# Kernel tuning notes

Hardware: AMD Instinct MI355X
Metric: run time of the kernel (lower is better)

The kernel has to match this reference:

```python
import jax, jax.numpy as jnp
import numpy as np

B = 16384
WIDE_DIM = 256          # 32 wide features * dim 8
DEEP_DIM = 1024         # 64 deep features * embedding_dim 16
SHARED = [2048, 1024, 512]
DOMAIN = [512, 256]
NUM_DOMAINS = 8


def setup_inputs() -> dict:
    key = jax.random.key(0)
    ks = jax.random.split(key, 20)
    s = 0.01  # embedding_init_var-style small init
    inp = {
        "wide_features": jax.random.normal(ks[0], (B, WIDE_DIM), jnp.float32),
        "deep_features": jax.random.normal(ks[1], (B, DEEP_DIM), jnp.float32),
        "domain_ids": jax.random.randint(ks[2], (B,), 0, NUM_DOMAINS, jnp.int64),
        # shared MLP (weights stored [in, out])
        "W1": jax.random.normal(ks[3], (DEEP_DIM, SHARED[0]), jnp.float32) * s,
        "b1": jnp.zeros((SHARED[0],), jnp.float32),
        "W2": jax.random.normal(ks[4], (SHARED[0], SHARED[1]), jnp.float32) * s,
        "b2": jnp.zeros((SHARED[1],), jnp.float32),
        "W3": jax.random.normal(ks[5], (SHARED[1], SHARED[2]), jnp.float32) * s,
        "b3": jnp.zeros((SHARED[2],), jnp.float32),
        # domain-specific MLP
        "Wd1": jax.random.normal(ks[6], (SHARED[2], DOMAIN[0]), jnp.float32) * s,
        "bd1": jnp.zeros((DOMAIN[0],), jnp.float32),
        "Wd2": jax.random.normal(ks[7], (DOMAIN[0], DOMAIN[1]), jnp.float32) * s,
        "bd2": jnp.zeros((DOMAIN[1],), jnp.float32),
        # per-domain output heads: Linear(DOMAIN[-1], 1) per domain
        "Wh": jax.random.normal(ks[8], (NUM_DOMAINS, DOMAIN[1]), jnp.float32) * s,
        "bh": jnp.zeros((NUM_DOMAINS,), jnp.float32),
    }
    return inp


def reference(wide_features, deep_features, domain_ids,
              W1, b1, W2, b2, W3, b3, Wd1, bd1, Wd2, bd2, Wh, bh):
    # wide part: sum embedding output to a scalar logit per sample [B, 1]
    wide = jnp.sum(wide_features, axis=1, keepdims=True)
    # shared deep MLP
    h = jax.nn.relu(deep_features @ W1 + b1)
    h = jax.nn.relu(h @ W2 + b2)
    shared = jax.nn.relu(h @ W3 + b3)          # [B, 512]
    # domain-specific tower (shared across domains)
    d = jax.nn.relu(shared @ Wd1 + bd1)
    d = jax.nn.relu(d @ Wd2 + bd2)             # [B, 256]
    # per-sample domain head routing: gather head weights, fused dot
    w = Wh[domain_ids]                          # [B, 256]
    head = jnp.sum(d * w, axis=1, keepdims=True) + bh[domain_ids][:, None]  # [B, 1]
    out = jax.nn.sigmoid(wide + head)
    return (out, shared, d)
```

## Files before the change

### kernel.cpp

```cpp
#include <hip/hip_runtime.h>
#include <hip/hip_bf16.h>


typedef __attribute__((ext_vector_type(8))) short short8;
typedef __attribute__((ext_vector_type(4))) float f32x4;

static __device__ __forceinline__ unsigned short f2bf_bits(float x) {
  __hip_bfloat16 h = __float2bfloat16(x);
  return __builtin_bit_cast(unsigned short, h);
}
static __device__ __forceinline__ float bf_bits2f(unsigned short u) {
  __hip_bfloat16 h = __builtin_bit_cast(__hip_bfloat16, u);
  return __bfloat162float(h);
}

static __device__ __forceinline__ void gload16(const void* g, void* l) {
  __builtin_amdgcn_global_load_lds(
      (const __attribute__((address_space(1))) void*)g,
      (__attribute__((address_space(3))) void*)l, 16, 0, 0);
}

#define MFMA16(a, b, c) __builtin_amdgcn_mfma_f32_16x16x32_bf16((a), (b), (c), 0, 0, 0)
#define SB0() __builtin_amdgcn_sched_barrier(0)
#define PRIO(x) __builtin_amdgcn_s_setprio(x)
#define BAR() __builtin_amdgcn_s_barrier()
#define MEMFENCE() asm volatile("" ::: "memory")

__global__ __launch_bounds__(256) void prep(
    const float* __restrict__ deep, unsigned short* __restrict__ deepb,
    const float* __restrict__ W1, __hip_bfloat16* __restrict__ W1t,
    const float* __restrict__ W2, __hip_bfloat16* __restrict__ W2t,
    const float* __restrict__ W3, __hip_bfloat16* __restrict__ W3t,
    const float* __restrict__ Wd1, __hip_bfloat16* __restrict__ Wd1t,
    const float* __restrict__ Wd2, __hip_bfloat16* __restrict__ Wd2t) {
  __shared__ float tile[64][65];
  int blk = blockIdx.x;
  if (blk < 8192) {
    int i = blk * 256 + threadIdx.x;
    const f32x4* p = (const f32x4*)deep + (size_t)i * 2;
    f32x4 a = p[0], b = p[1];
    short8 o;
    o[0] = (short)f2bf_bits(a[0]); o[1] = (short)f2bf_bits(a[1]);
    o[2] = (short)f2bf_bits(a[2]); o[3] = (short)f2bf_bits(a[3]);
    o[4] = (short)f2bf_bits(b[0]); o[5] = (short)f2bf_bits(b[1]);
    o[6] = (short)f2bf_bits(b[2]); o[7] = (short)f2bf_bits(b[3]);
    *(short8*)(deepb + (size_t)i * 8) = o;
    return;
  }
  blk -= 8192;
  const float* W; __hip_bfloat16* Wt; int K, N;
  if (blk < 512)       {             W = W1;  Wt = W1t;  K = 1024; N = 2048; }
  else if (blk < 1024) { blk -= 512;  W = W2;  Wt = W2t;  K = 2048; N = 1024; }
  else if (blk < 1152) { blk -= 1024; W = W3;  Wt = W3t;  K = 1024; N = 512; }
  else if (blk < 1216) { blk -= 1152; W = Wd1; Wt = Wd1t; K = 512;  N = 512; }
  else                 { blk -= 1216; W = Wd2; Wt = Wd2t; K = 512;  N = 256; }
  const int ntx = N >> 6;
  const int k0 = (blk / ntx) * 64;
  const int n0 = (blk % ntx) * 64;
  const int t  = threadIdx.x;
  const int tn = t & 63;
  const int t4 = t >> 6;
#pragma unroll
  for (int p = 0; p < 16; ++p) {
    int kl = p * 4 + t4;
    tile[kl][tn] = W[(size_t)(k0 + kl) * N + (n0 + tn)];
  }
  __syncthreads();
#pragma unroll
  for (int p = 0; p < 16; ++p) {
    int nl = p * 4 + t4;
    Wt[(size_t)(n0 + nl) * K + (k0 + tn)] = __float2bfloat16(tile[tn][nl]);
  }
}

__global__ __launch_bounds__(512, 2) void gemm_2c(
    const __hip_bfloat16* __restrict__ A,
    const __hip_bfloat16* __restrict__ Bt,
    const float* __restrict__ bias,
    __hip_bfloat16* __restrict__ Cb,
    float* __restrict__ Cf,
    int N, int K, int nbx) {
  __shared__ char lds[131072];

  const int tid  = threadIdx.x;
  const int lane = tid & 63;
  const int wid  = tid >> 6;
  const int wm   = wid >> 2;
  const int wn   = wid & 3;

  const int nwg = gridDim.x;
  const int cpx = nwg >> 3;
  const int id  = blockIdx.x;
  const int swz = (id & 7) * cpx + (id >> 3);
  const int bm  = (swz / nbx) * 256;
  const int bn  = (swz % nbx) * 256;

  const int ln15 = lane & 15;
  const unsigned aoff = (unsigned)((wm * 128 + ln15) * 128) +
                        (unsigned)((((lane >> 4) ^ (lane & 7)) << 4));
  const unsigned boff = 32768u + (unsigned)((wn * 64 + ln15) * 128) +
                        (unsigned)((((lane >> 4) ^ (lane & 7)) << 4));

  const int nt = K >> 6;

  const __hip_bfloat16* baseA = A  + (size_t)(bm + (tid >> 3)) * K +
                                ((tid & 7) ^ ((tid >> 3) & 7)) * 8;
  const __hip_bfloat16* baseB = Bt + (size_t)(bn + (tid >> 3)) * K +
                                ((tid & 7) ^ ((tid >> 3) & 7)) * 8;
  const unsigned ldst0 = (unsigned)(wid * 1024);

  auto stage = [&](int kt, int half, int isB) {
    const __hip_bfloat16* base = isB ? baseB : baseA;
    char* dst = lds + ((kt & 1) * 65536) + (isB ? 32768 : 0) + half * 16384;
#pragma unroll
    for (int q = 0; q < 2; ++q) {
      gload16(base + (size_t)((half * 128 + q * 64) * K + kt * 64),
              dst + q * 8192 + ldst0);
    }
  };

  auto LD = [&](unsigned off) -> short8 {
    return *(const short8*)&lds[off];
  };

  f32x4 acc[8][4] = {};
  short8 aLo[4][2], aHi[4][2], b0v[2][2], b1v[2][2];

  stage(0, 0, 1); stage(0, 1, 1); stage(0, 0, 0); stage(0, 1, 0);
  if (nt > 1) {
    stage(1, 0, 1); stage(1, 1, 1); stage(1, 0, 0); stage(1, 1, 0);
    asm volatile("s_waitcnt vmcnt(8)");
  } else {
    asm volatile("s_waitcnt vmcnt(0)");
  }
  BAR();
  MEMFENCE();
#pragma unroll
  for (int mi = 0; mi < 4; ++mi)
#pragma unroll
    for (int kk = 0; kk < 2; ++kk)
      aLo[mi][kk] = LD((aoff + (unsigned)(mi * 2048)) ^ (unsigned)(kk << 6));
#pragma unroll
  for (int nj = 0; nj < 2; ++nj)
#pragma unroll
    for (int kk = 0; kk < 2; ++kk)
      b0v[nj][kk] = LD((boff + (unsigned)(nj * 2048)) ^ (unsigned)(kk << 6));

  for (int t = 0; t < nt; ++t) {
    const unsigned po = (unsigned)(t & 1) * 65536u;
    const unsigned pn = po ^ 65536u;

#pragma unroll
    for (int nj = 0; nj < 2; ++nj)
#pragma unroll
      for (int kk = 0; kk < 2; ++kk)
        b1v[nj][kk] = LD((po + boff + (unsigned)((nj + 2) * 2048)) ^ (unsigned)(kk << 6));
    PRIO(1);
#pragma unroll
    for (int kk = 0; kk < 2; ++kk)
#pragma unroll
      for (int mi = 0; mi < 4; ++mi)
#pragma unroll
        for (int nj = 0; nj < 2; ++nj)
          acc[mi][nj] = MFMA16(aLo[mi][kk], b0v[nj][kk], acc[mi][nj]);
    PRIO(0);

#pragma unroll
    for (int mi = 0; mi < 4; ++mi)
#pragma unroll
      for (int kk = 0; kk < 2; ++kk)
        aHi[mi][kk] = LD((po + aoff + (unsigned)((mi + 4) * 2048)) ^ (unsigned)(kk << 6));
    PRIO(1);
#pragma unroll
    for (int kk = 0; kk < 2; ++kk)
#pragma unroll
      for (int mi = 0; mi < 4; ++mi)
#pragma unroll
        for (int nj = 0; nj < 2; ++nj)
          acc[mi][nj + 2] = MFMA16(aLo[mi][kk], b1v[nj][kk], acc[mi][nj + 2]);
    PRIO(0);
    BAR();
    MEMFENCE();

    PRIO(1);
#pragma unroll
    for (int kk = 0; kk < 2; ++kk)
#pragma unroll
      for (int mi = 0; mi < 4; ++mi)
#pragma unroll
        for (int nj = 0; nj < 2; ++nj)
          acc[mi + 4][nj] = MFMA16(aHi[mi][kk], b0v[nj][kk], acc[mi + 4][nj]);
    PRIO(0);
    if (t + 2 < nt) { stage(t + 2, 0, 1); stage(t + 2, 1, 1); }
    if (t + 1 < nt) {
      if (t + 2 < nt) asm volatile("s_waitcnt vmcnt(4)");
      else            asm volatile("s_waitcnt vmcnt(0)");
      BAR();
      MEMFENCE();
    }

    if (t + 1 < nt) {
#pragma unroll
      for (int mi = 0; mi < 4; ++mi)
#pragma unroll
        for (int kk = 0; kk < 2; ++kk)
          aLo[mi][kk] = LD((pn + aoff + (unsigned)(mi * 2048)) ^ (unsigned)(kk << 6));
#pragma unroll
      for (int nj = 0; nj < 2; ++nj)
#pragma unroll
        for (int kk = 0; kk < 2; ++kk)
          b0v[nj][kk] = LD((pn + boff + (unsigned)(nj * 2048)) ^ (unsigned)(kk << 6));
    }
    PRIO(1);
#pragma unroll
    for (int kk = 0; kk < 2; ++kk)
#pragma unroll
      for (int mi = 0; mi < 4; ++mi)
#pragma unroll
        for (int nj = 0; nj < 2; ++nj)
          acc[mi + 4][nj + 2] = MFMA16(aHi[mi][kk], b1v[nj][kk], acc[mi + 4][nj + 2]);
    PRIO(0);
    if (t + 2 < nt) { stage(t + 2, 0, 0); stage(t + 2, 1, 0); }
  }

  float biasv[4];
#pragma unroll
  for (int nj = 0; nj < 4; ++nj)
    biasv[nj] = bias[bn + wn * 64 + nj * 16 + ln15];

#pragma unroll
  for (int mi = 0; mi < 8; ++mi) {
    int row0 = bm + wm * 128 + mi * 16 + (lane >> 4) * 4;
#pragma unroll
    for (int nj = 0; nj < 4; ++nj) {
      int col = bn + wn * 64 + nj * 16 + ln15;
#pragma unroll
      for (int r = 0; r < 4; ++r) {
        float v = acc[mi][nj][r] + biasv[nj];
        v = v > 0.f ? v : 0.f;
        size_t idx = (size_t)(row0 + r) * N + col;
        Cb[idx] = __float2bfloat16(v);
        if (Cf) Cf[idx] = v;
      }
    }
  }
}

__global__ __launch_bounds__(512, 2) void tower(
    const __hip_bfloat16* __restrict__ H2,
    const __hip_bfloat16* __restrict__ W3t, const float* __restrict__ b3,
    const __hip_bfloat16* __restrict__ Wd1t, const float* __restrict__ bd1,
    const __hip_bfloat16* __restrict__ Wd2t, const float* __restrict__ bd2,
    float* __restrict__ Sf, float* __restrict__ Df,
    const float* __restrict__ wide, const int* __restrict__ dom,
    const float* __restrict__ Wh, const float* __restrict__ bh,
    float* __restrict__ outp) {
  __shared__ char lds[139264];
  const int tid  = threadIdx.x;
  const int lane = tid & 63;
  const int wid  = tid >> 6;
  const int ln15 = lane & 15;
  const int kq   = lane >> 4;

  const int id  = blockIdx.x;
  const int swz = (id & 7) * 32 + (id >> 3);
  const int bm  = swz * 64;

  const unsigned csel = (unsigned)(((unsigned)kq ^ (unsigned)((ln15 >> 1) & 3)) << 4);
  const int sc   = (tid & 3) ^ ((tid >> 3) & 3);
  const int srow = tid >> 2;

  auto LD = [&](unsigned off) -> short8 { return *(const short8*)&lds[off]; };

  auto stage3 = [&](int kt) {
    int half = kt & 1;
#pragma unroll
    for (int q = 0; q < 4; ++q)
      gload16(W3t + (size_t)(q * 128 + srow) * 1024 + kt * 32 + sc * 8,
              lds + 73728 + half * 32768 + q * 8192 + tid * 16);
    if (tid < 256)
      gload16(H2 + (size_t)(bm + srow) * 1024 + kt * 32 + sc * 8,
              lds + 65536 + half * 4096 + tid * 16);
  };

  f32x4 acc3[4][4] = {};
  stage3(0);
  for (int t = 0; t < 32; ++t) {
    if (t + 1 < 32) {
      stage3(t + 1);
      if (wid < 4) asm volatile("s_waitcnt vmcnt(5)");
      else         asm volatile("s_waitcnt vmcnt(4)");
    } else {
      asm volatile("s_waitcnt vmcnt(0)");
    }
    BAR(); MEMFENCE();
    const unsigned pa = 65536u + (unsigned)((t & 1) * 4096);
    const unsigned pb = 73728u + (unsigned)((t & 1) * 32768);
    short8 aF[4], bF[4];
#pragma unroll
    for (int mi = 0; mi < 4; ++mi)
      aF[mi] = LD(pa + (unsigned)((mi * 16 + ln15) * 64) + csel);
#pragma unroll
    for (int nj = 0; nj < 4; ++nj)
      bF[nj] = LD(pb + (unsigned)((wid * 64 + nj * 16 + ln15) * 64) + csel);
    PRIO(1);
#pragma unroll
    for (int mi = 0; mi < 4; ++mi)
#pragma unroll
      for (int nj = 0; nj < 4; ++nj)
        acc3[mi][nj] = MFMA16(aF[mi], bF[nj], acc3[mi][nj]);
    PRIO(0);
    BAR(); MEMFENCE();
  }

  {
    float bv[4];
#pragma unroll
    for (int nj = 0; nj < 4; ++nj) bv[nj] = b3[wid * 64 + nj * 16 + ln15];
#pragma unroll
    for (int mi = 0; mi < 4; ++mi) {
      int lrow = mi * 16 + kq * 4;
#pragma unroll
      for (int nj = 0; nj < 4; ++nj) {
        int col = wid * 64 + nj * 16 + ln15;
#pragma unroll
        for (int r = 0; r < 4; ++r) {
          float v = acc3[mi][nj][r] + bv[nj];
          v = v > 0.f ? v : 0.f;
          Sf[(size_t)(bm + lrow + r) * 512 + col] = v;
          int rr = lrow + r;
          *(unsigned short*)&lds[rr * 1024 + (((col >> 3) ^ (rr & 7)) << 4) +
                                 (col & 7) * 2] = f2bf_bits(v);
        }
      }
    }
  }

  auto stage4 = [&](int kt) {
    int half = kt & 1;
#pragma unroll
    for (int q = 0; q < 4; ++q)
      gload16(Wd1t + (size_t)(q * 128 + srow) * 512 + kt * 32 + sc * 8,
              lds + 73728 + half * 32768 + q * 8192 + tid * 16);
  };
  stage4(0);
  asm volatile("s_waitcnt lgkmcnt(0)");
  BAR(); MEMFENCE();

  f32x4 acc4[4][4] = {};
  for (int t = 0; t < 16; ++t) {
    if (t + 1 < 16) { stage4(t + 1); asm volatile("s_waitcnt vmcnt(4)"); }
    else            { asm volatile("s_waitcnt vmcnt(0)"); }
    BAR(); MEMFENCE();
    const unsigned pb = 73728u + (unsigned)((t & 1) * 32768);
    short8 aF[4], bF[4];
#pragma unroll
    for (int mi = 0; mi < 4; ++mi) {
      int rr = mi * 16 + ln15;
      aF[mi] = LD((unsigned)(rr * 1024) +
                  (unsigned)((((t * 4 + kq) ^ (rr & 7)) << 4)));
    }
#pragma unroll
    for (int nj = 0; nj < 4; ++nj)
      bF[nj] = LD(pb + (unsigned)((wid * 64 + nj * 16 + ln15) * 64) + csel);
    PRIO(1);
#pragma unroll
    for (int mi = 0; mi < 4; ++mi)
#pragma unroll
      for (int nj = 0; nj < 4; ++nj)
        acc4[mi][nj] = MFMA16(aF[mi], bF[nj], acc4[mi][nj]);
    PRIO(0);
    BAR(); MEMFENCE();
  }

  {
    float bv[4];
#pragma unroll
    for (int nj = 0; nj < 4; ++nj) bv[nj] = bd1[wid * 64 + nj * 16 + ln15];
#pragma unroll
    for (int mi = 0; mi < 4; ++mi) {
      int lrow = mi * 16 + kq * 4;
#pragma unroll
      for (int nj = 0; nj < 4; ++nj) {
        int col = wid * 64 + nj * 16 + ln15;
#pragma unroll
        for (int r = 0; r < 4; ++r) {
          float v = acc4[mi][nj][r] + bv[nj];
          v = v > 0.f ? v : 0.f;
          int rr = lrow + r;
          *(unsigned short*)&lds[rr * 1024 + (((col >> 3) ^ (rr & 7)) << 4) +
                                 (col & 7) * 2] = f2bf_bits(v);
        }
      }
    }
  }

  auto stage5 = [&](int kt) {
    int half = kt & 1;
#pragma unroll
    for (int q = 0; q < 2; ++q)
      gload16(Wd2t + (size_t)(q * 128 + srow) * 512 + kt * 32 + sc * 8,
              lds + 73728 + half * 16384 + q * 8192 + tid * 16);
  };
  stage5(0);
  asm volatile("s_waitcnt lgkmcnt(0)");
  BAR(); MEMFENCE();

  f32x4 acc5[4][2] = {};
  for (int t = 0; t < 16; ++t) {
    if (t + 1 < 16) { stage5(t + 1); asm volatile("s_waitcnt vmcnt(2)"); }
    else            { asm volatile("s_waitcnt vmcnt(0)"); }
    BAR(); MEMFENCE();
    const unsigned pb = 73728u + (unsigned)((t & 1) * 16384);
    short8 aF[4], bF[2];
#pragma unroll
    for (int mi = 0; mi < 4; ++mi) {
      int rr = mi * 16 + ln15;
      aF[mi] = LD((unsigned)(rr * 1024) +
                  (unsigned)((((t * 4 + kq) ^ (rr & 7)) << 4)));
    }
#pragma unroll
    for (int nj = 0; nj < 2; ++nj)
      bF[nj] = LD(pb + (unsigned)((wid * 32 + nj * 16 + ln15) * 64) + csel);
    PRIO(1);
#pragma unroll
    for (int mi = 0; mi < 4; ++mi)
#pragma unroll
      for (int nj = 0; nj < 2; ++nj)
        acc5[mi][nj] = MFMA16(aF[mi], bF[nj], acc5[mi][nj]);
    PRIO(0);
    BAR(); MEMFENCE();
  }

  unsigned short* ldsD = (unsigned short*)(lds + 65536);
  {
    float bv[2];
#pragma unroll
    for (int nj = 0; nj < 2; ++nj) bv[nj] = bd2[wid * 32 + nj * 16 + ln15];
#pragma unroll
    for (int mi = 0; mi < 4; ++mi) {
      int lrow = mi * 16 + kq * 4;
#pragma unroll
      for (int nj = 0; nj < 2; ++nj) {
        int col = wid * 32 + nj * 16 + ln15;
#pragma unroll
        for (int r = 0; r < 4; ++r) {
          float v = acc5[mi][nj][r] + bv[nj];
          v = v > 0.f ? v : 0.f;
          Df[(size_t)(bm + lrow + r) * 256 + col] = v;
          ldsD[(lrow + r) * 264 + col] = f2bf_bits(v);
        }
      }
    }
  }
  asm volatile("s_waitcnt lgkmcnt(0)");
  BAR(); MEMFENCE();

  const int hrow = tid >> 3;
  const int he   = tid & 7;
  float s = 0.f;
  {
    const f32x4* wp = (const f32x4*)(wide + (size_t)(bm + hrow) * 256 + he * 32);
#pragma unroll
    for (int j = 0; j < 8; ++j) {
      f32x4 w = wp[j];
      s += w[0] + w[1] + w[2] + w[3];
    }
  }
  const int dm = dom[bm + hrow];
  {
    const f32x4* hp = (const f32x4*)(Wh + (size_t)dm * 256 + he * 32);
    const short8* dp = (const short8*)(ldsD + hrow * 264 + he * 32);
#pragma unroll
    for (int j = 0; j < 4; ++j) {
      short8 d8 = dp[j];
      f32x4 h0 = hp[2 * j], h1 = hp[2 * j + 1];
      s += bf_bits2f((unsigned short)d8[0]) * h0[0] +
           bf_bits2f((unsigned short)d8[1]) * h0[1] +
           bf_bits2f((unsigned short)d8[2]) * h0[2] +
           bf_bits2f((unsigned short)d8[3]) * h0[3] +
           bf_bits2f((unsigned short)d8[4]) * h1[0] +
           bf_bits2f((unsigned short)d8[5]) * h1[1] +
           bf_bits2f((unsigned short)d8[6]) * h1[2] +
           bf_bits2f((unsigned short)d8[7]) * h1[3];
    }
  }
  float* ldsH = (float*)(lds + 100352);
  ldsH[hrow * 8 + he] = s;
  asm volatile("s_waitcnt lgkmcnt(0)");
  BAR(); MEMFENCE();

  if (tid < 64) {
    float v = 0.f;
#pragma unroll
    for (int j = 0; j < 8; ++j) v += ldsH[tid * 8 + j];
    int dmr = dom[bm + tid];
    float x = v + bh[dmr];
    outp[bm + tid] = 1.f / (1.f + __expf(-x));
  }
}

extern "C" void kernel_launch(void* const* d_in, const int* in_sizes, int n_in,
                              void* d_out, int out_size, void* d_ws, size_t ws_size,
                              hipStream_t stream) {
  const float* wide = (const float*)d_in[0];
  const float* deep = (const float*)d_in[1];
  const int*   dom  = (const int*)d_in[2];
  const float* W1  = (const float*)d_in[3];
  const float* b1  = (const float*)d_in[4];
  const float* W2  = (const float*)d_in[5];
  const float* b2  = (const float*)d_in[6];
  const float* W3  = (const float*)d_in[7];
  const float* b3  = (const float*)d_in[8];
  const float* Wd1 = (const float*)d_in[9];
  const float* bd1 = (const float*)d_in[10];
  const float* Wd2 = (const float*)d_in[11];
  const float* bd2 = (const float*)d_in[12];
  const float* Wh  = (const float*)d_in[13];
  const float* bh  = (const float*)d_in[14];
  float* out = (float*)d_out;

  const int B = 16384;
  char* ws = (char*)d_ws;
  __hip_bfloat16* buf0 = (__hip_bfloat16*)ws;
  __hip_bfloat16* buf1 = (__hip_bfloat16*)(ws + 33554432ull);
  __hip_bfloat16* W1t  = (__hip_bfloat16*)(ws + 100663296ull);
  __hip_bfloat16* W2t  = W1t + 2048 * 1024;
  __hip_bfloat16* W3t  = W2t + 1024 * 2048;
  __hip_bfloat16* Wd1t = W3t + 512 * 1024;
  __hip_bfloat16* Wd2t = Wd1t + 512 * 512;

  prep<<<dim3(8192 + 1248), 256, 0, stream>>>(
      deep, (unsigned short*)buf0, W1, W1t, W2, W2t, W3, W3t, Wd1, Wd1t, Wd2, Wd2t);

  float* shared_out = out + B;
  float* d_out_f    = out + B + (size_t)B * 512;

  gemm_2c<<<dim3((2048 / 256) * (B / 256)), 512, 0, stream>>>(
      buf0, W1t, b1, buf1, nullptr, 2048, 1024, 2048 / 256);
  gemm_2c<<<dim3((1024 / 256) * (B / 256)), 512, 0, stream>>>(
      buf1, W2t, b2, buf0, nullptr, 1024, 2048, 1024 / 256);
  tower<<<dim3(256), 512, 0, stream>>>(
      buf0, W3t, b3, Wd1t, bd1, Wd2t, bd2,
      shared_out, d_out_f, wide, dom, Wh, bh, out);
}
```

Measured before the change: 200.7 us.

## Add 128x256-tile double-buffered GEMM kernel for first shared layer

New measurement: 210.7 us. 5.0% more time.

```diff
diff --git a/kernel.cpp b/kernel.cpp
--- a/kernel.cpp
+++ b/kernel.cpp
@@ -21,7 +21,6 @@
 }
 
 #define MFMA16(a, b, c) __builtin_amdgcn_mfma_f32_16x16x32_bf16((a), (b), (c), 0, 0, 0)
-#define SB0() __builtin_amdgcn_sched_barrier(0)
 #define PRIO(x) __builtin_amdgcn_s_setprio(x)
 #define BAR() __builtin_amdgcn_s_barrier()
 #define MEMFENCE() asm volatile("" ::: "memory")
@@ -73,6 +72,104 @@
   }
 }
 
+__global__ __launch_bounds__(256, 2) void gemm_hi(
+    const __hip_bfloat16* __restrict__ A,
+    const __hip_bfloat16* __restrict__ Bt,
+    const float* __restrict__ bias,
+    __hip_bfloat16* __restrict__ Cb,
+    float* __restrict__ Cf,
+    int N, int K, int nbx) {
+  __shared__ char lds[49152];
+
+  const int tid  = threadIdx.x;
+  const int lane = tid & 63;
+  const int wid  = tid >> 6;
+  const int wmr  = wid >> 1;
+  const int wnc  = wid & 1;
+
+  const int nwg = gridDim.x;
+  const int cpx = nwg >> 3;
+  const int id  = blockIdx.x;
+  const int swz = (id & 7) * cpx + (id >> 3);
+  const int bm  = (swz / nbx) * 128;
+  const int bn  = (swz % nbx) * 256;
+
+  const int ln15 = lane & 15;
+  const int kq   = lane >> 4;
+  const unsigned csel = (unsigned)(((unsigned)kq ^ (unsigned)((ln15 >> 1) & 3)) << 4);
+
+  const int srow = tid >> 2;
+  const int sc   = (tid & 3) ^ ((tid >> 3) & 3);
+  const __hip_bfloat16* baseA = A  + (size_t)(bm + srow) * K + sc * 8;
+  const __hip_bfloat16* baseB = Bt + (size_t)(bn + srow) * K + sc * 8;
+
+  const int nt = K >> 5;
+
+  auto stage = [&](int kt) {
+    char* dst = lds + (kt & 1) * 24576;
+#pragma unroll
+    for (int q = 0; q < 2; ++q)
+      gload16(baseA + (size_t)((q * 64) * K + kt * 32), dst + q * 4096 + tid * 16);
+#pragma unroll
+    for (int q = 0; q < 4; ++q)
+      gload16(baseB + (size_t)((q * 64) * K + kt * 32),
+              dst + 8192 + q * 4096 + tid * 16);
+  };
+
+  auto LD = [&](unsigned off) -> short8 { return *(const short8*)&lds[off]; };
+
+  f32x4 acc[4][8] = {};
+
+  stage(0);
+  for (int t = 0; t < nt; ++t) {
+    if (t + 1 < nt) {
+      stage(t + 1);
+      asm volatile("s_waitcnt vmcnt(6)");
+    } else {
+      asm volatile("s_waitcnt vmcnt(0)");
+    }
+    BAR(); MEMFENCE();
+    const unsigned pb = (unsigned)((t & 1) * 24576);
+    short8 aF[4], bF[8];
+#pragma unroll
+    for (int mi = 0; mi < 4; ++mi)
+      aF[mi] = LD(pb + (unsigned)((wmr * 64 + mi * 16 + ln15) * 64) + csel);
+#pragma unroll
+    for (int nj = 0; nj < 8; ++nj)
+      bF[nj] = LD(pb + 8192u + (unsigned)((wnc * 128 + nj * 16 + ln15) * 64) + csel);
+    PRIO(1);
+#pragma unroll
+    for (int mi = 0; mi < 4; ++mi)
+#pragma unroll
+      for (int nj = 0; nj < 8; ++nj)
+        acc[mi][nj] = MFMA16(aF[mi], bF[nj], acc[mi][nj]);
+    PRIO(0);
+    BAR(); MEMFENCE();
+  }
+
+  float biasv[8];
+#pragma unroll
+  for (int nj = 0; nj < 8; ++nj)
+    biasv[nj] = bias[bn + wnc * 128 + nj * 16 + ln15];
+
+#pragma unroll
+  for (int mi = 0; mi < 4; ++mi) {
+    int row0 = bm + wmr * 64 + mi * 16 + kq * 4;
+#pragma unroll
+    for (int nj = 0; nj < 8; ++nj) {
+      int col = bn + wnc * 128 + nj * 16 + ln15;
+#pragma unroll
+      for (int r = 0; r < 4; ++r) {
+        float v = acc[mi][nj][r] + biasv[nj];
+        v = v > 0.f ? v : 0.f;
+        size_t idx = (size_t)(row0 + r) * N + col;
+        Cb[idx] = __float2bfloat16(v);
+        if (Cf) Cf[idx] = v;
+      }
+    }
+  }
+}
+
 __global__ __launch_bounds__(512, 2) void gemm_2c(
     const __hip_bfloat16* __restrict__ A,
     const __hip_bfloat16* __restrict__ Bt,
@@ -536,7 +633,7 @@
   float* shared_out = out + B;
   float* d_out_f    = out + B + (size_t)B * 512;
 
-  gemm_2c<<<dim3((2048 / 256) * (B / 256)), 512, 0, stream>>>(
+  gemm_hi<<<dim3((B / 128) * (2048 / 256)), 256, 0, stream>>>(
       buf0, W1t, b1, buf1, nullptr, 2048, 1024, 2048 / 256);
   gemm_2c<<<dim3((1024 / 256) * (B / 256)), 512, 0, stream>>>(
       buf1, W2t, b2, buf0, nullptr, 1024, 2048, 1024 / 256);
```
